# Kernel optimization log

Hardware: AMD Instinct MI355X
Metric: run time of the kernel (lower is better)

Reference implementation:

```python
import jax, jax.numpy as jnp
import numpy as np

C = 64; K = 3; KS = 7; A = 16
B, H, W = 4, 128, 128
EXTEND_SCOPE = 1.0
EPS = 1e-5

def _dct_mats(n):
    k = np.arange(n)[:, None]; m = np.arange(n)[None, :]
    D = 2.0 * np.cos(np.pi * (2 * m + 1) * k / (2.0 * n))  # torch_dct DCT-II, norm=None
    return jnp.asarray(D, jnp.float32), jnp.asarray(np.linalg.inv(D), jnp.float32)

_D, _Dinv = _dct_mats(K)

def _conv2d(x, w, b=None, stride=(1, 1), padding='SAME', groups=1):
    y = jax.lax.conv_general_dilated(x, w, stride, padding, feature_group_count=groups, dimension_numbers=('NCHW', 'OIHW', 'NCHW'))
    return y if b is None else y + b[None, :, None, None]

def _dwt(x):
    x1 = x[:, :, 0::2, 0::2] * 0.5; x2 = x[:, :, 1::2, 0::2] * 0.5
    x3 = x[:, :, 0::2, 1::2] * 0.5; x4 = x[:, :, 1::2, 1::2] * 0.5
    return (x1 + x2 + x3 + x4, -x1 + x2 - x3 + x4, -x1 - x2 + x3 + x4, x1 - x2 - x3 + x4)

def _iwt(LL, LH, HL, HH):
    a, b_, c, d = LL * 0.5, LH * 0.5, HL * 0.5, HH * 0.5
    n, ch, h, w = LL.shape
    out = jnp.zeros((n, ch, 2 * h, 2 * w), LL.dtype)
    out = out.at[:, :, 0::2, 0::2].set(a - b_ - c + d)
    out = out.at[:, :, 1::2, 0::2].set(a + b_ - c - d)
    out = out.at[:, :, 0::2, 1::2].set(a - b_ + c - d)
    out = out.at[:, :, 1::2, 1::2].set(a + b_ + c + d)
    return out

def _omni(x, fc_w, bn_g, bn_b, bn_m, bn_v, ch_w, ch_b, fl_w, fl_b, sp_w=None, sp_b=None):
    g = x.mean((2, 3))                                   # global avg pool -> [B,C]
    a = g @ fc_w.T
    a = jax.nn.relu((a - bn_m) * jax.lax.rsqrt(bn_v + EPS) * bn_g + bn_b)  # BN (eval)
    c_att = jax.nn.sigmoid(a @ ch_w.T + ch_b)
    f_att = jax.nn.sigmoid(a @ fl_w.T + fl_b)
    sp_att = None if sp_w is None else jax.nn.sigmoid(a @ sp_w.T + sp_b)
    return c_att, f_att, sp_att

def _forward(x, weight, ratio, o1_fc_w, o1_bn_g, o1_bn_b, o1_bn_m, o1_bn_v, o1_ch_w, o1_ch_b, o1_fl_w, o1_fl_b, o2_fc_w, o2_bn_g, o2_bn_b, o2_bn_m, o2_bn_v, o2_ch_w, o2_ch_b, o2_fl_w, o2_fl_b, o2_sp_w, o2_sp_b, off_w, off_b, obn_g, obn_b, obn_m, obn_v, ds_w, ds_b, gn_g, gn_b):
    b = x.shape[0]
    LL, LH, HL, HH = _dwt(x)
    c1, f1, _ = _omni(x, o1_fc_w, o1_bn_g, o1_bn_b, o1_bn_m, o1_bn_v, o1_ch_w, o1_ch_b, o1_fl_w, o1_fl_b)
    c2, f2, sp2 = _omni(x, o2_fc_w, o2_bn_g, o2_bn_b, o2_bn_m, o2_bn_v, o2_ch_w, o2_ch_b, o2_fl_w, o2_fl_b, o2_sp_w, o2_sp_b)
    # adaptive frequency-modulated dynamic kernels
    aw = jnp.broadcast_to(weight[None], (b,) + weight.shape)        # [B,Co,Ci,K,K]
    awm = aw.mean((-1, -2), keepdims=True)
    awr = aw - awm
    dctc = jnp.einsum('km,bojmn,ln->bojkl', _D, awr, _D)            # dct_2d
    dctc = dctc * (sp2.reshape(b, 1, 1, K, K) * 2.0)
    awr = jnp.einsum('km,bojmn,ln->bojkl', _Dinv, dctc, _Dinv)      # idct_2d
    aw = ratio * (awm * (c1[:, None, :, None, None] * 2) * (f1[:, :, None, None, None] * 2)) + (1.0 - ratio) * (awr * (c2[:, None, :, None, None] * 2) * (f2[:, :, None, None, None] * 2))
    # grouped conv (groups=b*C) then sum over c_in == depthwise conv with kernels summed over c_in (Cin==Cout)
    weff = aw.sum(axis=2)                                           # [B,C,K,K]
    h2, w2 = HH.shape[2], HH.shape[3]
    hh = _conv2d(HH.reshape(1, b * C, h2, w2), weff.reshape(b * C, 1, K, K), groups=b * C).reshape(b, C, h2, w2)
    out = _iwt(LL, LH, HL, hh) + x
    # ---- DSConv (dynamic snake conv, morph=0) ----
    off = _conv2d(out, off_w, off_b)
    off = (off - obn_m[None, :, None, None]) * jax.lax.rsqrt(obn_v + EPS)[None, :, None, None] * obn_g[None, :, None, None] + obn_b[None, :, None, None]
    y_off = jnp.tanh(off)[:, :KS]                                   # [B,KS,H,W]
    center = KS // 2
    low = jnp.flip(jnp.cumsum(jnp.flip(y_off[:, :center], 1), 1), 1)
    up = jnp.cumsum(y_off[:, center + 1:], 1)
    dy = jnp.concatenate([low, jnp.zeros_like(y_off[:, :1]), up], 1) * EXTEND_SCOPE
    hh_, ww_ = out.shape[2], out.shape[3]
    rows = jnp.clip(jnp.arange(hh_, dtype=x.dtype)[None, None, :, None] + dy, 0.0, hh_ - 1.0)
    cols = jnp.arange(ww_, dtype=x.dtype)[None, None, None, :] + (jnp.arange(KS, dtype=x.dtype) - center)[None, :, None, None]
    cols = jnp.clip(jnp.broadcast_to(cols, rows.shape), 0.0, ww_ - 1.0)
    r0 = jnp.floor(rows); c0 = jnp.floor(cols)
    wr = (rows - r0)[:, None]; wc = (cols - c0)[:, None]            # [B,1,KS,H,W]
    r0i = r0.astype(jnp.int32); c0i = c0.astype(jnp.int32)
    r1i = jnp.minimum(r0i + 1, hh_ - 1); c1i = jnp.minimum(c0i + 1, ww_ - 1)
    samp = jax.vmap(lambda img, ri, ci: img[:, ri, ci])             # [C,H,W],[KS,H,W] -> [C,KS,H,W]
    g00 = samp(out, r0i, c0i); g01 = samp(out, r0i, c1i)
    g10 = samp(out, r1i, c0i); g11 = samp(out, r1i, c1i)
    deform = (1 - wr) * (1 - wc) * g00 + (1 - wr) * wc * g01 + wr * (1 - wc) * g10 + wr * wc * g11
    deform = deform.transpose(0, 1, 3, 2, 4).reshape(b, C, hh_ * KS, ww_)
    y = _conv2d(deform, ds_w, ds_b, stride=(KS, 1), padding='VALID')  # [B,C,H,W]
    G = C // 4                                                       # GroupNorm(out//4)
    z = y.reshape(b, G, C // G, hh_, ww_)
    mu = z.mean((2, 3, 4), keepdims=True)
    var = ((z - mu) ** 2).mean((2, 3, 4), keepdims=True)
    y = ((z - mu) * jax.lax.rsqrt(var + EPS)).reshape(b, C, hh_, ww_)
    return jax.nn.relu(y * gn_g[None, :, None, None] + gn_b[None, :, None, None])

def setup_inputs() -> dict:
    key = jax.random.key(0)
    ks = jax.random.split(key, 12)
    def n(k, shape, s): return jax.random.normal(k, shape, jnp.float32) * s
    return dict(
        x=jax.random.normal(ks[0], (B, C, H, W), jnp.float32),
        weight=n(ks[1], (C, C, K, K), 0.1),
        ratio=jnp.asarray(0.5, jnp.float32),
        o1_fc_w=n(ks[2], (A, C), 0.2), o1_bn_g=jnp.ones((A,), jnp.float32), o1_bn_b=jnp.zeros((A,), jnp.float32),
        o1_bn_m=jnp.zeros((A,), jnp.float32), o1_bn_v=jnp.ones((A,), jnp.float32),
        o1_ch_w=n(ks[3], (C, A), 0.2), o1_ch_b=jnp.zeros((C,), jnp.float32),
        o1_fl_w=n(ks[4], (C, A), 0.2), o1_fl_b=jnp.zeros((C,), jnp.float32),
        o2_fc_w=n(ks[5], (A, C), 0.2), o2_bn_g=jnp.ones((A,), jnp.float32), o2_bn_b=jnp.zeros((A,), jnp.float32),
        o2_bn_m=jnp.zeros((A,), jnp.float32), o2_bn_v=jnp.ones((A,), jnp.float32),
        o2_ch_w=n(ks[6], (C, A), 0.2), o2_ch_b=jnp.zeros((C,), jnp.float32),
        o2_fl_w=n(ks[7], (C, A), 0.2), o2_fl_b=jnp.zeros((C,), jnp.float32),
        o2_sp_w=n(ks[8], (K * K, A), 0.2), o2_sp_b=jnp.zeros((K * K,), jnp.float32),
        off_w=n(ks[9], (2 * KS, C, 3, 3), 0.05), off_b=jnp.zeros((2 * KS,), jnp.float32),
        obn_g=jnp.ones((2 * KS,), jnp.float32), obn_b=jnp.zeros((2 * KS,), jnp.float32),
        obn_m=jnp.zeros((2 * KS,), jnp.float32), obn_v=jnp.ones((2 * KS,), jnp.float32),
        ds_w=n(ks[10], (C, C, KS, 1), 0.05), ds_b=jnp.zeros((C,), jnp.float32),
        gn_g=jnp.ones((C,), jnp.float32), gn_b=jnp.zeros((C,), jnp.float32),
    )

def reference(x, weight, ratio, o1_fc_w, o1_bn_g, o1_bn_b, o1_bn_m, o1_bn_v, o1_ch_w, o1_ch_b, o1_fl_w, o1_fl_b, o2_fc_w, o2_bn_g, o2_bn_b, o2_bn_m, o2_bn_v, o2_ch_w, o2_ch_b, o2_fl_w, o2_fl_b, o2_sp_w, o2_sp_b, off_w, off_b, obn_g, obn_b, obn_m, obn_v, ds_w, ds_b, gn_g, gn_b):
    return _forward(x, weight, ratio, o1_fc_w, o1_bn_g, o1_bn_b, o1_bn_m, o1_bn_v, o1_ch_w, o1_ch_b, o1_fl_w, o1_fl_b, o2_fc_w, o2_bn_g, o2_bn_b, o2_bn_m, o2_bn_v, o2_ch_w, o2_ch_b, o2_fl_w, o2_fl_b, o2_sp_w, o2_sp_b, off_w, off_b, obn_g, obn_b, obn_m, obn_v, ds_w, ds_b, gn_g, gn_b)
```

## Files before the change

### kernel.cpp

```cpp
#include <hip/hip_runtime.h>
#include <math.h>

#define BB 4
#define CC 64
#define HH_ 128
#define WW 128
#define HPW (HH_*WW)
#define KH 64
#define KW 64
#define KSZ 7
#define AA 16
#define EPSV 1e-5f
#define KTOT 448

typedef __attribute__((ext_vector_type(8))) short bf16x8;
typedef __attribute__((ext_vector_type(4))) float f32x4;
typedef unsigned short ushort_t;

__device__ __forceinline__ float sigm(float x){ return 1.0f/(1.0f+expf(-x)); }
__device__ __forceinline__ unsigned short f2bf(float f){
  unsigned u = __float_as_uint(f);
  return (unsigned short)((u + 0x7fffu + ((u>>16)&1u)) >> 16);
}

__global__ __launch_bounds__(512) void k_dwt0(const float* __restrict__ x,
  const float* __restrict__ dsw, const float* __restrict__ offw,
  float* __restrict__ HHb, float* __restrict__ partial,
  ushort_t* __restrict__ dsWbf, ushort_t* __restrict__ offAbf)
{
  int t = threadIdx.x; int wg = blockIdx.x;
  int idx = wg*512 + t;
  if(idx < CC*KTOT){
    int co = idx/KTOT; int K = idx%KTOT; int k = K>>6; int ci = K&63;
    dsWbf[idx] = f2bf(dsw[(size_t)(co*CC+ci)*KSZ + k]);
  } else {
    int j2 = idx - CC*KTOT;
    if(j2 < 18*16*32){
      int kl = j2&31; int co = (j2>>5)&15; int s = j2>>9;
      int tap = s>>1; int ci = (s&1)*32 + kl;
      float v = 0.f;
      if(co<KSZ) v = offw[((size_t)co*CC + ci)*9 + tap];
      offAbf[j2] = f2bf(v);
    }
  }
  int lane = t&63, wid = t>>6;
  int e0 = wg*2048 + t*4;
  int bc = e0>>12; int h2 = (e0>>6)&63; int w0 = e0&63;
  const float* xp = x + (size_t)bc*HPW;
  float4 a0 = *(const float4*)(xp + (2*h2)*WW + 2*w0);
  float4 a1 = *(const float4*)(xp + (2*h2)*WW + 2*w0 + 4);
  float4 b0 = *(const float4*)(xp + (2*h2+1)*WW + 2*w0);
  float4 b1 = *(const float4*)(xp + (2*h2+1)*WW + 2*w0 + 4);
  float4 hh;
  hh.x = 0.5f*(a0.x - b0.x - a0.y + b0.y);
  hh.y = 0.5f*(a0.z - b0.z - a0.w + b0.w);
  hh.z = 0.5f*(a1.x - b1.x - a1.y + b1.y);
  hh.w = 0.5f*(a1.z - b1.z - a1.w + b1.w);
  *(float4*)(HHb + e0) = hh;
  float s = a0.x+a0.y+a0.z+a0.w + a1.x+a1.y+a1.z+a1.w
          + b0.x+b0.y+b0.z+b0.w + b1.x+b1.y+b1.z+b1.w;
  for(int o=32;o>0;o>>=1) s += __shfl_down(s,o);
  __shared__ float ls[8];
  if(lane==0) ls[wid] = s;
  __syncthreads();
  if(t==0){
    float tot=0.f;
    #pragma unroll
    for(int k2=0;k2<8;k2++) tot += ls[k2];
    partial[wg] = tot;
  }
}

__global__ __launch_bounds__(64) void k_weff2(const float* __restrict__ partial,
  const float* __restrict__ w, const float* __restrict__ ratio_p,
  const float* __restrict__ o1fc, const float* __restrict__ o1g,const float* __restrict__ o1b,
  const float* __restrict__ o1m,const float* __restrict__ o1v,
  const float* __restrict__ o1cw,const float* __restrict__ o1cb,
  const float* __restrict__ o1fw,const float* __restrict__ o1fb,
  const float* __restrict__ o2fc, const float* __restrict__ o2g,const float* __restrict__ o2b,
  const float* __restrict__ o2m,const float* __restrict__ o2v,
  const float* __restrict__ o2cw,const float* __restrict__ o2cb,
  const float* __restrict__ o2fw,const float* __restrict__ o2fb,
  const float* __restrict__ spw,const float* __restrict__ spb,
  float* __restrict__ weff)
{
  int bo = blockIdx.x; int b = bo>>6, o = bo&63; int ci = threadIdx.x;
  int bc = b*CC+ci;
  float g_own = (partial[2*bc] + partial[2*bc+1]) * (1.0f/HPW);
  float d1=o1cb[ci], d2=o1fb[ci], d3=o2cb[ci], d4=o2fb[ci];
  float sspacc[9];
  #pragma unroll
  for(int e=0;e<9;e++) sspacc[e]=spb[e];
  for(int j=0;j<AA;j++){
    float p1 = g_own * o1fc[j*CC+ci];
    float p2 = g_own * o2fc[j*CC+ci];
    #pragma unroll
    for(int off=32;off>0;off>>=1){ p1+=__shfl_xor(p1,off); p2+=__shfl_xor(p2,off); }
    p1 = (p1-o1m[j])*rsqrtf(o1v[j]+EPSV)*o1g[j]+o1b[j]; p1=fmaxf(p1,0.f);
    p2 = (p2-o2m[j])*rsqrtf(o2v[j]+EPSV)*o2g[j]+o2b[j]; p2=fmaxf(p2,0.f);
    d1 += p1*o1cw[ci*AA+j]; d2 += p1*o1fw[ci*AA+j];
    d3 += p2*o2cw[ci*AA+j]; d4 += p2*o2fw[ci*AA+j];
    #pragma unroll
    for(int e=0;e<9;e++) sspacc[e] += p2*spw[e*AA+j];
  }
  float sc1v=sigm(d1), sc2v=sigm(d3);
  float sf1o=__shfl(sigm(d2),o), sf2o=__shfl(sigm(d4),o);
  const float* wp = w + (size_t)(o*CC+ci)*9;
  float w9[9]; float m=0.f;
  #pragma unroll
  for(int e=0;e<9;e++){ w9[e]=wp[e]; m+=w9[e]; }
  m *= (1.0f/9.0f);
  float S1 = m * sc1v;
  float M[9];
  #pragma unroll
  for(int e=0;e<9;e++) M[e] = (w9[e]-m)*sc2v;
  #pragma unroll
  for(int off=32; off>0; off>>=1){
    S1 += __shfl_xor(S1, off);
    #pragma unroll
    for(int e=0;e<9;e++) M[e] += __shfl_xor(M[e], off);
  }
  if(ci==0){
    const float Dm[3][3] = {{2.f,2.f,2.f},{1.7320508075688772f,0.f,-1.7320508075688772f},{1.f,-2.f,1.f}};
    const float Di[3][3] = {{0.16666666666666666f,0.28867513459481287f,0.16666666666666666f},
                            {0.16666666666666666f,0.f,-0.3333333333333333f},
                            {0.16666666666666666f,-0.28867513459481287f,0.16666666666666666f}};
    float U[3][3], T[3][3], V[3][3], R[3][3];
    for(int k=0;k<3;k++)for(int n=0;n<3;n++) U[k][n]=Dm[k][0]*M[0*3+n]+Dm[k][1]*M[1*3+n]+Dm[k][2]*M[2*3+n];
    for(int k=0;k<3;k++)for(int l=0;l<3;l++) T[k][l]=(U[k][0]*Dm[l][0]+U[k][1]*Dm[l][1]+U[k][2]*Dm[l][2])*2.0f*sigm(sspacc[k*3+l]);
    for(int k=0;k<3;k++)for(int n=0;n<3;n++) V[k][n]=Di[k][0]*T[0][n]+Di[k][1]*T[1][n]+Di[k][2]*T[2][n];
    for(int k=0;k<3;k++)for(int l=0;l<3;l++) R[k][l]=V[k][0]*Di[l][0]+V[k][1]*Di[l][1]+V[k][2]*Di[l][2];
    float rr = ratio_p[0];
    float base = rr*4.0f*sf1o*S1;
    float w2f = (1.0f-rr)*4.0f*sf2o;
    #pragma unroll
    for(int e=0;e<9;e++) weff[(size_t)bo*9+e] = base + w2f*R[e/3][e%3];
  }
}

__global__ __launch_bounds__(256) void k_iwtT(const float* __restrict__ HHb,
  const float* __restrict__ x, const float* __restrict__ weff,
  float* __restrict__ outT, ushort_t* __restrict__ outTbf)
{
  __shared__ __align__(16) char smem[33024 + 16640];
  float* hs  = (float*)smem;
  float* xt  = (float*)smem;
  float* d_s = (float*)(smem + 33024);
  int wg = blockIdx.x; int b = wg>>7, h = wg&127; int h2 = h>>1;
  int t = threadIdx.x;
  #pragma unroll
  for(int half=0; half<2; ++half){
    for(int e=t; e<32*3*66; e+=256){
      int c_l = e/198; int rem = e - c_l*198; int r3 = rem/66; int wz = rem - r3*66;
      int r = h2 - 1 + r3; int w2 = wz - 1;
      int c = half*32 + c_l;
      float v = 0.f;
      if(r>=0 && r<KH && w2>=0 && w2<KW)
        v = HHb[((size_t)(b*CC+c))*(KH*KW) + r*KW + w2];
      hs[(c_l*3 + r3)*66 + wz] = v;
    }
    __syncthreads();
    {
      int c_l = t>>3, q = t&7;
      int c = half*32 + c_l;
      float wk[9];
      #pragma unroll
      for(int e=0;e<9;e++) wk[e] = weff[(size_t)(b*CC+c)*9+e];
      const float* hb = hs + c_l*198;
      #pragma unroll
      for(int j=0;j<8;j++){
        int w2 = q*8+j;
        float conv = 0.f;
        #pragma unroll
        for(int dh=0;dh<3;dh++){
          const float* hr = hb + dh*66 + w2;
          conv += wk[dh*3+0]*hr[0] + wk[dh*3+1]*hr[1] + wk[dh*3+2]*hr[2];
        }
        d_s[c*65+w2] = 0.5f*(conv - hb[1*66 + w2 + 1]);
      }
    }
    __syncthreads();
  }
  for(int e=t; e<CC*WW; e+=256){
    int cc=e>>7, w=e&127;
    xt[cc*129+w] = x[((size_t)(b*CC+cc)*HH_+h)*WW + w];
  }
  __syncthreads();
  float* dst = outT + ((size_t)(b*HH_+h))*WW*CC;
  ushort_t* dstb = outTbf + ((size_t)(b*HH_+h))*130*CC;
  for(int e=t; e<CC*WW; e+=256){
    int w=e>>6, cc=e&63;
    float dv = d_s[cc*65+(w>>1)];
    float val = 2.f*xt[cc*129+w] + (((h + w)&1) ? -dv : dv);
    dst[e] = val;
    dstb[(w+1)*CC + cc] = f2bf(val);
  }
  if(t<128){ int cc=t&63; int side=t>>6; dstb[(size_t)side*129*CC + cc] = 0; }
}

__global__ __launch_bounds__(512) void k_dsfused(const float* __restrict__ outT,
  const ushort_t* __restrict__ outTbf, const ushort_t* __restrict__ dsWbf,
  const ushort_t* __restrict__ offAbf, const float* __restrict__ offb,
  const float* __restrict__ obg, const float* __restrict__ obb,
  const float* __restrict__ obm, const float* __restrict__ obv,
  const float* __restrict__ dsb, float* __restrict__ yout, float* __restrict__ pstats)
{
  __shared__ ushort_t S2a[2*8192];
  __shared__ int sb0[KSZ*128], sb1[KSZ*128];
  __shared__ float swr[KSZ*128];
  __shared__ float off_s[KSZ*128];
  __shared__ float dy_s[KSZ*128];
  int t = threadIdx.x;
  int wg = blockIdx.x; int sw = (wg&7)*64 + (wg>>3);
  int b = sw>>7, h = sw&127;
  int lane = t&63, wid = t>>6;
  int arow = lane&15, kgrp = lane>>4;
  {
    f32x4 acc = (f32x4){0.f,0.f,0.f,0.f};
    #pragma unroll
    for(int s=0;s<18;s++){
      int tap = s>>1, chalf = s&1;
      int r = tap/3, dwp = tap%3;
      int hr = h - 1 + r;
      if(hr<0 || hr>=HH_) continue;
      bf16x8 aF = *(const bf16x8*)(offAbf + (s*16+arow)*32 + kgrp*8);
      const ushort_t* base = outTbf + ((size_t)(b*HH_+hr))*130*CC + chalf*32 + kgrp*8;
      int wp = (wid<<4) + arow + dwp;
      bf16x8 bF = *(const bf16x8*)(base + (size_t)wp*CC);
      acc = __builtin_amdgcn_mfma_f32_16x16x32_bf16(aF, bF, acc, 0,0,0);
    }
    #pragma unroll
    for(int r=0;r<4;r++){
      int co = kgrp*4+r;
      if(co<KSZ) off_s[co*128 + (wid<<4) + arow] = acc[r];
    }
  }
  __syncthreads();
  if(t<128){
    int w = t;
    float y[KSZ];
    #pragma unroll
    for(int k=0;k<KSZ;k++){
      float sc = obg[k]*rsqrtf(obv[k]+EPSV);
      float sh = obb[k]-obm[k]*sc;
      y[k] = tanhf((off_s[k*128+w]+offb[k])*sc+sh);
    }
    dy_s[      w]=y[0]+y[1]+y[2]; dy_s[128+w]=y[1]+y[2]; dy_s[256+w]=y[2];
    dy_s[384+w]=0.f; dy_s[512+w]=y[4]; dy_s[640+w]=y[4]+y[5]; dy_s[768+w]=y[4]+y[5]+y[6];
  }
  __syncthreads();
  for(int e=t; e<KSZ*128; e+=512){
    int k = e>>7, w = e&127;
    float dv = dy_s[e];
    float r = fminf(fmaxf((float)h + dv, 0.f), 127.f);
    float rf = floorf(r); int r0=(int)rf; float wr=r-rf; int r1=min(r0+1,127);
    int c = min(max(w+k-3,0),127);
    sb0[k*128+w] = ((b*HH_+r0)*WW+c)*CC;
    sb1[k*128+w] = ((b*HH_+r1)*WW+c)*CC;
    swr[k*128+w] = wr;
  }
  __syncthreads();
  int cg2 = wid&3, wh = wid>>2;
  {
    ushort_t* buf = S2a;
    #pragma unroll
    for(int i=0;i<16;i++){
      int p = (wid<<4)+i;
      int b0=sb0[p], b1=sb1[p]; float wr=swr[p];
      float av = outT[b0+lane], c2 = outT[b1+lane];
      float v = av + wr*(c2-av);
      int idx = (p<<6)|lane;
      buf[idx ^ ((p&7)<<3)] = f2bf(v);
    }
  }
  __syncthreads();
  f32x4 acc[4];
  #pragma unroll
  for(int nt=0;nt<4;nt++) acc[nt] = (f32x4){0.f,0.f,0.f,0.f};
  int bufs = 0;
  for(int k=0;k<KSZ;k++){
    const ushort_t* Wp = dsWbf + (size_t)((cg2<<4)+arow)*KTOT + (k<<6) + kgrp*8;
    bf16x8 a0 = *(const bf16x8*)Wp;
    bf16x8 a1 = *(const bf16x8*)(Wp+32);
    if(k+1<KSZ){
      ushort_t* nb = S2a + (bufs^1)*8192;
      #pragma unroll
      for(int i=0;i<16;i++){
        int p = (wid<<4)+i;
        int b0=sb0[(k+1)*128+p], b1=sb1[(k+1)*128+p]; float wr=swr[(k+1)*128+p];
        float av = outT[b0+lane], c2 = outT[b1+lane];
        float v = av + wr*(c2-av);
        int idx = (p<<6)|lane;
        nb[idx ^ ((p&7)<<3)] = f2bf(v);
      }
    }
    const ushort_t* cb = S2a + bufs*8192;
    #pragma unroll
    for(int nt=0;nt<4;nt++){
      int pos = (wh<<6) + (nt<<4) + arow;
      int i0 = (pos<<6) + kgrp*8;
      int sz = (pos&7)<<3;
      bf16x8 b0 = *(const bf16x8*)(cb + (i0 ^ sz));
      bf16x8 b1 = *(const bf16x8*)(cb + ((i0+32) ^ sz));
      acc[nt] = __builtin_amdgcn_mfma_f32_16x16x32_bf16(a0, b0, acc[nt], 0,0,0);
      acc[nt] = __builtin_amdgcn_mfma_f32_16x16x32_bf16(a1, b1, acc[nt], 0,0,0);
    }
    __syncthreads();
    bufs ^= 1;
  }
  float vs[4]={0.f,0.f,0.f,0.f}, vq[4]={0.f,0.f,0.f,0.f};
  #pragma unroll
  for(int r=0;r<4;r++){
    int co = (cg2<<4) + kgrp*4 + r;
    float bias = dsb[co];
    #pragma unroll
    for(int nt=0;nt<4;nt++){
      float y = acc[nt][r] + bias;
      int wcol = (wh<<6) + (nt<<4) + arow;
      yout[((size_t)(b*CC+co)*HH_ + h)*WW + wcol] = y;
      vs[r] += y; vq[r] += y*y;
    }
  }
  #pragma unroll
  for(int m=1;m<16;m<<=1){
    #pragma unroll
    for(int r=0;r<4;r++){ vs[r]+=__shfl_xor(vs[r],m); vq[r]+=__shfl_xor(vq[r],m); }
  }
  if(arow==0){
    #pragma unroll
    for(int r=0;r<4;r++){
      int co = (cg2<<4)+kgrp*4+r;
      int pi = (b*CC+co)*256 + h*2 + wh;
      pstats[pi] = vs[r];
      pstats[65536+pi] = vq[r];
    }
  }
}

__global__ __launch_bounds__(256) void k_gnfin2(const float* __restrict__ pstats,
                                                float* __restrict__ gstat){
  int bg = blockIdx.x; int b = bg>>4, g = bg&15; int t = threadIdx.x;
  float s=0.f, q=0.f;
  #pragma unroll
  for(int c4=0;c4<4;c4++){
    int base = (b*CC + g*4+c4)*256;
    s += pstats[base + t];
    q += pstats[65536 + base + t];
  }
  for(int o=32;o>0;o>>=1){ s+=__shfl_down(s,o); q+=__shfl_down(q,o); }
  __shared__ float ls[4], lq[4];
  if((t&63)==0){ ls[t>>6]=s; lq[t>>6]=q; }
  __syncthreads();
  if(t==0){
    float S=ls[0]+ls[1]+ls[2]+ls[3], Q=lq[0]+lq[1]+lq[2]+lq[3];
    float inv = 1.0f/(4.0f*HPW);
    float mu = S*inv; float var = Q*inv - mu*mu;
    gstat[bg*2]=mu; gstat[bg*2+1]=rsqrtf(var+EPSV);
  }
}

__global__ void k_gnapply(float* __restrict__ y, const float* __restrict__ gstat,
  const float* __restrict__ gg, const float* __restrict__ gb){
  int idx = blockIdx.x*256 + threadIdx.x;
  float4* p = (float4*)y;
  int bc = idx >> 12;
  int b = bc>>6, c = bc&63;
  int gi = b*16 + (c>>2);
  float mu = gstat[gi*2], rstd = gstat[gi*2+1];
  float sc = rstd*gg[c], sh = gb[c]-mu*sc;
  float4 v = p[idx];
  v.x = fmaxf(v.x*sc+sh, 0.f);
  v.y = fmaxf(v.y*sc+sh, 0.f);
  v.z = fmaxf(v.z*sc+sh, 0.f);
  v.w = fmaxf(v.w*sc+sh, 0.f);
  p[idx] = v;
}

extern "C" void kernel_launch(void* const* d_in, const int* in_sizes, int n_in,
                              void* d_out, int out_size, void* d_ws, size_t ws_size,
                              hipStream_t stream) {
  const float* x      = (const float*)d_in[0];
  const float* weight = (const float*)d_in[1];
  const float* ratio  = (const float*)d_in[2];
  const float* o1fc   = (const float*)d_in[3];
  const float* o1g    = (const float*)d_in[4];
  const float* o1b    = (const float*)d_in[5];
  const float* o1m    = (const float*)d_in[6];
  const float* o1v    = (const float*)d_in[7];
  const float* o1cw   = (const float*)d_in[8];
  const float* o1cb   = (const float*)d_in[9];
  const float* o1fw   = (const float*)d_in[10];
  const float* o1fb   = (const float*)d_in[11];
  const float* o2fc   = (const float*)d_in[12];
  const float* o2g    = (const float*)d_in[13];
  const float* o2b    = (const float*)d_in[14];
  const float* o2m    = (const float*)d_in[15];
  const float* o2v    = (const float*)d_in[16];
  const float* o2cw   = (const float*)d_in[17];
  const float* o2cb   = (const float*)d_in[18];
  const float* o2fw   = (const float*)d_in[19];
  const float* o2fb   = (const float*)d_in[20];
  const float* spw    = (const float*)d_in[21];
  const float* spb    = (const float*)d_in[22];
  const float* offw   = (const float*)d_in[23];
  const float* offb   = (const float*)d_in[24];
  const float* obg    = (const float*)d_in[25];
  const float* obb    = (const float*)d_in[26];
  const float* obm    = (const float*)d_in[27];
  const float* obv    = (const float*)d_in[28];
  const float* dsw    = (const float*)d_in[29];
  const float* dsb    = (const float*)d_in[30];
  const float* gng    = (const float*)d_in[31];
  const float* gnb    = (const float*)d_in[32];

  float* ws    = (float*)d_ws;
  float* HHb   = ws;
  float* partial = ws + 1048576;
  float* weff  = ws + 1049088;
  float* gstat = ws + 1051392;
  ushort_t* dsWbf  = (ushort_t*)(ws + 1051520);
  ushort_t* offAbf = (ushort_t*)(ws + 1065856);
  float* pstats= ws + 1070464;
  float* outT  = ws + 1201536;
  ushort_t* outTbf = (ushort_t*)(ws + 5395840);
  float* outb  = (float*)d_out;

  k_dwt0<<<512,512,0,stream>>>(x, dsw, offw, HHb, partial, dsWbf, offAbf);
  k_weff2<<<256,64,0,stream>>>(partial, weight, ratio,
    o1fc,o1g,o1b,o1m,o1v,o1cw,o1cb,o1fw,o1fb,
    o2fc,o2g,o2b,o2m,o2v,o2cw,o2cb,o2fw,o2fb,
    spw,spb, weff);
  k_iwtT<<<512,256,0,stream>>>(HHb, x, weff, outT, outTbf);
  k_dsfused<<<512,512,0,stream>>>(outT, outTbf, dsWbf, offAbf,
    offb, obg, obb, obm, obv, dsb, outb, pstats);
  k_gnfin2<<<64,256,0,stream>>>(pstats, gstat);
  k_gnapply<<<4096,256,0,stream>>>(outb, gstat, gng, gnb);
}
```

Measured before the change: 95.87 us.

## Share IWT row pair per block and prefetch gathers into registers across MFMA

k_iwtT now handles both output rows that share one half-resolution HH row, so the 3x3 conv on HH is computed once per pair instead of twice, and the grid is halved. In k_dsfused, all 14 weight fragments are loaded into registers up front. The next tap's gathered outT values are issued as register loads before the MFMA block and only interpolated and written to LDS afterwards, so global load latency overlaps with matrix math. In exchange, register pressure rises (aF[14], L0/L1[16]) under a 512-thread launch bound that now also requests 4 blocks.

Result: slower. 101.9 us (+6.3%).

```diff
diff --git a/kernel.cpp b/kernel.cpp
--- a/kernel.cpp
+++ b/kernel.cpp
@@ -146,7 +146,7 @@
   float* hs  = (float*)smem;
   float* xt  = (float*)smem;
   float* d_s = (float*)(smem + 33024);
-  int wg = blockIdx.x; int b = wg>>7, h = wg&127; int h2 = h>>1;
+  int wg = blockIdx.x; int b = wg>>6, h2 = wg&63;
   int t = threadIdx.x;
   #pragma unroll
   for(int half=0; half<2; ++half){
@@ -181,24 +181,29 @@
     }
     __syncthreads();
   }
-  for(int e=t; e<CC*WW; e+=256){
-    int cc=e>>7, w=e&127;
-    xt[cc*129+w] = x[((size_t)(b*CC+cc)*HH_+h)*WW + w];
-  }
-  __syncthreads();
-  float* dst = outT + ((size_t)(b*HH_+h))*WW*CC;
-  ushort_t* dstb = outTbf + ((size_t)(b*HH_+h))*130*CC;
-  for(int e=t; e<CC*WW; e+=256){
-    int w=e>>6, cc=e&63;
-    float dv = d_s[cc*65+(w>>1)];
-    float val = 2.f*xt[cc*129+w] + (((h + w)&1) ? -dv : dv);
-    dst[e] = val;
-    dstb[(w+1)*CC + cc] = f2bf(val);
-  }
-  if(t<128){ int cc=t&63; int side=t>>6; dstb[(size_t)side*129*CC + cc] = 0; }
-}
-
-__global__ __launch_bounds__(512) void k_dsfused(const float* __restrict__ outT,
+  #pragma unroll
+  for(int r=0;r<2;r++){
+    int h = 2*h2 + r;
+    for(int e=t; e<CC*WW; e+=256){
+      int cc=e>>7, w=e&127;
+      xt[cc*129+w] = x[((size_t)(b*CC+cc)*HH_+h)*WW + w];
+    }
+    __syncthreads();
+    float* dst = outT + ((size_t)(b*HH_+h))*WW*CC;
+    ushort_t* dstb = outTbf + ((size_t)(b*HH_+h))*130*CC;
+    for(int e=t; e<CC*WW; e+=256){
+      int w=e>>6, cc=e&63;
+      float dv = d_s[cc*65+(w>>1)];
+      float val = 2.f*xt[cc*129+w] + (((h + w)&1) ? -dv : dv);
+      dst[e] = val;
+      dstb[(w+1)*CC + cc] = f2bf(val);
+    }
+    if(t<128){ int cc=t&63; int side=t>>6; dstb[(size_t)side*129*CC + cc] = 0; }
+    __syncthreads();
+  }
+}
+
+__global__ __launch_bounds__(512,4) void k_dsfused(const float* __restrict__ outT,
   const ushort_t* __restrict__ outTbf, const ushort_t* __restrict__ dsWbf,
   const ushort_t* __restrict__ offAbf, const float* __restrict__ offb,
   const float* __restrict__ obg, const float* __restrict__ obb,
@@ -261,17 +266,22 @@
   }
   __syncthreads();
   int cg2 = wid&3, wh = wid>>2;
+  int pbase = wid<<4;
+  bf16x8 aF[14];
   {
-    ushort_t* buf = S2a;
-    #pragma unroll
-    for(int i=0;i<16;i++){
-      int p = (wid<<4)+i;
-      int b0=sb0[p], b1=sb1[p]; float wr=swr[p];
-      float av = outT[b0+lane], c2 = outT[b1+lane];
-      float v = av + wr*(c2-av);
-      int idx = (p<<6)|lane;
-      buf[idx ^ ((p&7)<<3)] = f2bf(v);
-    }
+    const ushort_t* Wp = dsWbf + (size_t)((cg2<<4)+arow)*KTOT + kgrp*8;
+    #pragma unroll
+    for(int ks=0;ks<14;ks++) aF[ks] = *(const bf16x8*)(Wp + ks*32);
+  }
+  float L0[16], L1[16];
+  #pragma unroll
+  for(int i=0;i<16;i++){ int p=pbase+i; L0[i]=outT[sb0[p]+lane]; L1[i]=outT[sb1[p]+lane]; }
+  #pragma unroll
+  for(int i=0;i<16;i++){
+    int p=pbase+i;
+    float v = L0[i] + swr[p]*(L1[i]-L0[i]);
+    int idx=(p<<6)|lane;
+    S2a[idx ^ ((p&7)<<3)] = f2bf(v);
   }
   __syncthreads();
   f32x4 acc[4];
@@ -279,19 +289,11 @@
   for(int nt=0;nt<4;nt++) acc[nt] = (f32x4){0.f,0.f,0.f,0.f};
   int bufs = 0;
   for(int k=0;k<KSZ;k++){
-    const ushort_t* Wp = dsWbf + (size_t)((cg2<<4)+arow)*KTOT + (k<<6) + kgrp*8;
-    bf16x8 a0 = *(const bf16x8*)Wp;
-    bf16x8 a1 = *(const bf16x8*)(Wp+32);
     if(k+1<KSZ){
-      ushort_t* nb = S2a + (bufs^1)*8192;
       #pragma unroll
       for(int i=0;i<16;i++){
-        int p = (wid<<4)+i;
-        int b0=sb0[(k+1)*128+p], b1=sb1[(k+1)*128+p]; float wr=swr[(k+1)*128+p];
-        float av = outT[b0+lane], c2 = outT[b1+lane];
-        float v = av + wr*(c2-av);
-        int idx = (p<<6)|lane;
-        nb[idx ^ ((p&7)<<3)] = f2bf(v);
+        int e=(k+1)*128 + pbase + i;
+        L0[i]=outT[sb0[e]+lane]; L1[i]=outT[sb1[e]+lane];
       }
     }
     const ushort_t* cb = S2a + bufs*8192;
@@ -302,8 +304,18 @@
       int sz = (pos&7)<<3;
       bf16x8 b0 = *(const bf16x8*)(cb + (i0 ^ sz));
       bf16x8 b1 = *(const bf16x8*)(cb + ((i0+32) ^ sz));
-      acc[nt] = __builtin_amdgcn_mfma_f32_16x16x32_bf16(a0, b0, acc[nt], 0,0,0);
-      acc[nt] = __builtin_amdgcn_mfma_f32_16x16x32_bf16(a1, b1, acc[nt], 0,0,0);
+      acc[nt] = __builtin_amdgcn_mfma_f32_16x16x32_bf16(aF[2*k], b0, acc[nt], 0,0,0);
+      acc[nt] = __builtin_amdgcn_mfma_f32_16x16x32_bf16(aF[2*k+1], b1, acc[nt], 0,0,0);
+    }
+    if(k+1<KSZ){
+      ushort_t* nb = S2a + (bufs^1)*8192;
+      #pragma unroll
+      for(int i=0;i<16;i++){
+        int p = pbase+i;
+        float v = L0[i] + swr[(k+1)*128+p]*(L1[i]-L0[i]);
+        int idx=(p<<6)|lane;
+        nb[idx ^ ((p&7)<<3)] = f2bf(v);
+      }
     }
     __syncthreads();
     bufs ^= 1;
@@ -430,7 +442,7 @@
     o1fc,o1g,o1b,o1m,o1v,o1cw,o1cb,o1fw,o1fb,
     o2fc,o2g,o2b,o2m,o2v,o2cw,o2cb,o2fw,o2fb,
     spw,spb, weff);
-  k_iwtT<<<512,256,0,stream>>>(HHb, x, weff, outT, outTbf);
+  k_iwtT<<<256,256,0,stream>>>(HHb, x, weff, outT, outTbf);
   k_dsfused<<<512,512,0,stream>>>(outT, outTbf, dsWbf, offAbf,
     offb, obg, obb, obm, obv, dsb, outb, pstats);
   k_gnfin2<<<64,256,0,stream>>>(pstats, gstat);
```

## Gather deformable samples directly into MFMA registers and halve iwt blocks

Applied to the files above, without the earlier changes.

The deformable-conv kernel no longer stages interpolated samples in a double-buffered LDS tile with barriers. Each wave now loads float4 vectors from outT for its own 16 columns, lerps them straight into bf16 MFMA B fragments, and loops over all four output-channel groups. This drops shared memory traffic and per-tap syncs, but each wave now reloads all the weight fragments and the partial-stats buffer grows fourfold. Separately, the iwt kernel handles two output rows per block, reusing the HH conv result (d_s) for both rows instead of recomputing it per row.

Result: slower. 135.5 us (+41.3%).

```diff
diff --git a/kernel.cpp b/kernel.cpp
--- a/kernel.cpp
+++ b/kernel.cpp
@@ -21,6 +21,18 @@
 __device__ __forceinline__ unsigned short f2bf(float f){
   unsigned u = __float_as_uint(f);
   return (unsigned short)((u + 0x7fffu + ((u>>16)&1u)) >> 16);
+}
+__device__ __forceinline__ bf16x8 lerp8(float4 a0, float4 a1, float4 b0, float4 b1, float wr){
+  bf16x8 r;
+  r[0]=(short)f2bf(a0.x + wr*(b0.x-a0.x));
+  r[1]=(short)f2bf(a0.y + wr*(b0.y-a0.y));
+  r[2]=(short)f2bf(a0.z + wr*(b0.z-a0.z));
+  r[3]=(short)f2bf(a0.w + wr*(b0.w-a0.w));
+  r[4]=(short)f2bf(a1.x + wr*(b1.x-a1.x));
+  r[5]=(short)f2bf(a1.y + wr*(b1.y-a1.y));
+  r[6]=(short)f2bf(a1.z + wr*(b1.z-a1.z));
+  r[7]=(short)f2bf(a1.w + wr*(b1.w-a1.w));
+  return r;
 }
 
 __global__ __launch_bounds__(512) void k_dwt0(const float* __restrict__ x,
@@ -146,7 +158,7 @@
   float* hs  = (float*)smem;
   float* xt  = (float*)smem;
   float* d_s = (float*)(smem + 33024);
-  int wg = blockIdx.x; int b = wg>>7, h = wg&127; int h2 = h>>1;
+  int wg = blockIdx.x; int b = wg>>6, h2 = wg&63;
   int t = threadIdx.x;
   #pragma unroll
   for(int half=0; half<2; ++half){
@@ -181,21 +193,26 @@
     }
     __syncthreads();
   }
-  for(int e=t; e<CC*WW; e+=256){
-    int cc=e>>7, w=e&127;
-    xt[cc*129+w] = x[((size_t)(b*CC+cc)*HH_+h)*WW + w];
-  }
-  __syncthreads();
-  float* dst = outT + ((size_t)(b*HH_+h))*WW*CC;
-  ushort_t* dstb = outTbf + ((size_t)(b*HH_+h))*130*CC;
-  for(int e=t; e<CC*WW; e+=256){
-    int w=e>>6, cc=e&63;
-    float dv = d_s[cc*65+(w>>1)];
-    float val = 2.f*xt[cc*129+w] + (((h + w)&1) ? -dv : dv);
-    dst[e] = val;
-    dstb[(w+1)*CC + cc] = f2bf(val);
-  }
-  if(t<128){ int cc=t&63; int side=t>>6; dstb[(size_t)side*129*CC + cc] = 0; }
+  #pragma unroll
+  for(int r=0;r<2;r++){
+    int h = 2*h2 + r;
+    for(int e=t; e<CC*WW; e+=256){
+      int cc=e>>7, w=e&127;
+      xt[cc*129+w] = x[((size_t)(b*CC+cc)*HH_+h)*WW + w];
+    }
+    __syncthreads();
+    float* dst = outT + ((size_t)(b*HH_+h))*WW*CC;
+    ushort_t* dstb = outTbf + ((size_t)(b*HH_+h))*130*CC;
+    for(int e=t; e<CC*WW; e+=256){
+      int w=e>>6, cc=e&63;
+      float dv = d_s[cc*65+(w>>1)];
+      float val = 2.f*xt[cc*129+w] + (((h + w)&1) ? -dv : dv);
+      dst[e] = val;
+      dstb[(w+1)*CC + cc] = f2bf(val);
+    }
+    if(t<128){ int cc=t&63; int side=t>>6; dstb[(size_t)side*129*CC + cc] = 0; }
+    __syncthreads();
+  }
 }
 
 __global__ __launch_bounds__(512) void k_dsfused(const float* __restrict__ outT,
@@ -205,7 +222,6 @@
   const float* __restrict__ obm, const float* __restrict__ obv,
   const float* __restrict__ dsb, float* __restrict__ yout, float* __restrict__ pstats)
 {
-  __shared__ ushort_t S2a[2*8192];
   __shared__ int sb0[KSZ*128], sb1[KSZ*128];
   __shared__ float swr[KSZ*128];
   __shared__ float off_s[KSZ*128];
@@ -260,79 +276,65 @@
     swr[k*128+w] = wr;
   }
   __syncthreads();
-  int cg2 = wid&3, wh = wid>>2;
-  {
-    ushort_t* buf = S2a;
-    #pragma unroll
-    for(int i=0;i<16;i++){
-      int p = (wid<<4)+i;
-      int b0=sb0[p], b1=sb1[p]; float wr=swr[p];
-      float av = outT[b0+lane], c2 = outT[b1+lane];
-      float v = av + wr*(c2-av);
-      int idx = (p<<6)|lane;
-      buf[idx ^ ((p&7)<<3)] = f2bf(v);
-    }
-  }
-  __syncthreads();
+  int w = (wid<<4) + arow;
   f32x4 acc[4];
   #pragma unroll
-  for(int nt=0;nt<4;nt++) acc[nt] = (f32x4){0.f,0.f,0.f,0.f};
-  int bufs = 0;
+  for(int cg=0;cg<4;cg++) acc[cg] = (f32x4){0.f,0.f,0.f,0.f};
+  #pragma unroll
   for(int k=0;k<KSZ;k++){
-    const ushort_t* Wp = dsWbf + (size_t)((cg2<<4)+arow)*KTOT + (k<<6) + kgrp*8;
-    bf16x8 a0 = *(const bf16x8*)Wp;
-    bf16x8 a1 = *(const bf16x8*)(Wp+32);
-    if(k+1<KSZ){
-      ushort_t* nb = S2a + (bufs^1)*8192;
+    int e = k*128 + w;
+    int b0 = sb0[e], b1 = sb1[e]; float wr = swr[e];
+    int off = kgrp*8;
+    const float* p0 = outT + b0 + off;
+    const float* p1 = outT + b1 + off;
+    const float* q0 = p0 + 32;
+    const float* q1 = p1 + 32;
+    float4 r0a = *(const float4*)(p0);
+    float4 r0b = *(const float4*)(p0+4);
+    float4 r1a = *(const float4*)(p1);
+    float4 r1b = *(const float4*)(p1+4);
+    float4 s0a = *(const float4*)(q0);
+    float4 s0b = *(const float4*)(q0+4);
+    float4 s1a = *(const float4*)(q1);
+    float4 s1b = *(const float4*)(q1+4);
+    bf16x8 bF0 = lerp8(r0a, r0b, r1a, r1b, wr);
+    bf16x8 bF1 = lerp8(s0a, s0b, s1a, s1b, wr);
+    #pragma unroll
+    for(int cg=0;cg<4;cg++){
+      const ushort_t* Wp = dsWbf + (size_t)((cg<<4)+arow)*KTOT + (k<<6) + kgrp*8;
+      bf16x8 a0 = *(const bf16x8*)Wp;
+      bf16x8 a1 = *(const bf16x8*)(Wp+32);
+      acc[cg] = __builtin_amdgcn_mfma_f32_16x16x32_bf16(a0, bF0, acc[cg], 0,0,0);
+      acc[cg] = __builtin_amdgcn_mfma_f32_16x16x32_bf16(a1, bF1, acc[cg], 0,0,0);
+    }
+  }
+  float vs[16], vq[16];
+  #pragma unroll
+  for(int cg=0;cg<4;cg++){
+    #pragma unroll
+    for(int r=0;r<4;r++){
+      int co = (cg<<4) + kgrp*4 + r;
+      float y = acc[cg][r] + dsb[co];
+      int wcol = (wid<<4) + arow;
+      yout[((size_t)(b*CC+co)*HH_ + h)*WW + wcol] = y;
+      vs[cg*4+r] = y; vq[cg*4+r] = y*y;
+    }
+  }
+  #pragma unroll
+  for(int m=1;m<16;m<<=1){
+    #pragma unroll
+    for(int i=0;i<16;i++){ vs[i]+=__shfl_xor(vs[i],m); vq[i]+=__shfl_xor(vq[i],m); }
+  }
+  if(arow==0){
+    #pragma unroll
+    for(int cg=0;cg<4;cg++){
       #pragma unroll
-      for(int i=0;i<16;i++){
-        int p = (wid<<4)+i;
-        int b0=sb0[(k+1)*128+p], b1=sb1[(k+1)*128+p]; float wr=swr[(k+1)*128+p];
-        float av = outT[b0+lane], c2 = outT[b1+lane];
-        float v = av + wr*(c2-av);
-        int idx = (p<<6)|lane;
-        nb[idx ^ ((p&7)<<3)] = f2bf(v);
+      for(int r=0;r<4;r++){
+        int co = (cg<<4)+kgrp*4+r;
+        int pi = (b*CC+co)*1024 + h*8 + wid;
+        pstats[pi] = vs[cg*4+r];
+        pstats[262144+pi] = vq[cg*4+r];
       }
-    }
-    const ushort_t* cb = S2a + bufs*8192;
-    #pragma unroll
-    for(int nt=0;nt<4;nt++){
-      int pos = (wh<<6) + (nt<<4) + arow;
-      int i0 = (pos<<6) + kgrp*8;
-      int sz = (pos&7)<<3;
-      bf16x8 b0 = *(const bf16x8*)(cb + (i0 ^ sz));
-      bf16x8 b1 = *(const bf16x8*)(cb + ((i0+32) ^ sz));
-      acc[nt] = __builtin_amdgcn_mfma_f32_16x16x32_bf16(a0, b0, acc[nt], 0,0,0);
-      acc[nt] = __builtin_amdgcn_mfma_f32_16x16x32_bf16(a1, b1, acc[nt], 0,0,0);
-    }
-    __syncthreads();
-    bufs ^= 1;
-  }
-  float vs[4]={0.f,0.f,0.f,0.f}, vq[4]={0.f,0.f,0.f,0.f};
-  #pragma unroll
-  for(int r=0;r<4;r++){
-    int co = (cg2<<4) + kgrp*4 + r;
-    float bias = dsb[co];
-    #pragma unroll
-    for(int nt=0;nt<4;nt++){
-      float y = acc[nt][r] + bias;
-      int wcol = (wh<<6) + (nt<<4) + arow;
-      yout[((size_t)(b*CC+co)*HH_ + h)*WW + wcol] = y;
-      vs[r] += y; vq[r] += y*y;
-    }
-  }
-  #pragma unroll
-  for(int m=1;m<16;m<<=1){
-    #pragma unroll
-    for(int r=0;r<4;r++){ vs[r]+=__shfl_xor(vs[r],m); vq[r]+=__shfl_xor(vq[r],m); }
-  }
-  if(arow==0){
-    #pragma unroll
-    for(int r=0;r<4;r++){
-      int co = (cg2<<4)+kgrp*4+r;
-      int pi = (b*CC+co)*256 + h*2 + wh;
-      pstats[pi] = vs[r];
-      pstats[65536+pi] = vq[r];
     }
   }
 }
@@ -343,9 +345,11 @@
   float s=0.f, q=0.f;
   #pragma unroll
   for(int c4=0;c4<4;c4++){
-    int base = (b*CC + g*4+c4)*256;
-    s += pstats[base + t];
-    q += pstats[65536 + base + t];
+    int base = (b*CC + g*4+c4)*1024;
+    for(int i=t;i<1024;i+=256){
+      s += pstats[base + i];
+      q += pstats[262144 + base + i];
+    }
   }
   for(int o=32;o>0;o>>=1){ s+=__shfl_down(s,o); q+=__shfl_down(q,o); }
   __shared__ float ls[4], lq[4];
@@ -421,8 +425,8 @@
   ushort_t* dsWbf  = (ushort_t*)(ws + 1051520);
   ushort_t* offAbf = (ushort_t*)(ws + 1065856);
   float* pstats= ws + 1070464;
-  float* outT  = ws + 1201536;
-  ushort_t* outTbf = (ushort_t*)(ws + 5395840);
+  float* outT  = ws + 1594752;
+  ushort_t* outTbf = (ushort_t*)(ws + 5789056);
   float* outb  = (float*)d_out;
 
   k_dwt0<<<512,512,0,stream>>>(x, dsw, offw, HHb, partial, dsWbf, offAbf);
@@ -430,7 +434,7 @@
     o1fc,o1g,o1b,o1m,o1v,o1cw,o1cb,o1fw,o1fb,
     o2fc,o2g,o2b,o2m,o2v,o2cw,o2cb,o2fw,o2fb,
     spw,spb, weff);
-  k_iwtT<<<512,256,0,stream>>>(HHb, x, weff, outT, outTbf);
+  k_iwtT<<<256,256,0,stream>>>(HHb, x, weff, outT, outTbf);
   k_dsfused<<<512,512,0,stream>>>(outT, outTbf, dsWbf, offAbf,
     offb, obg, obb, obm, obv, dsb, outb, pstats);
   k_gnfin2<<<64,256,0,stream>>>(pstats, gstat);
```

## Split deformable-conv blocks by width half and share HH-conv across row pairs

Applied to the files above, without the earlier changes.

k_iwtT now handles two output rows per block, so the 3x3 conv on the half-resolution HH band is computed once and reused for both rows instead of being recomputed. k_dsfused is split into 1024 blocks of 256 threads, each covering a 64-column half-row with 4 waves that each own 16 output channels, and it preloads all 14 weight fragments into registers before the k-loop. The aim is to remove redundant conv work, raise block count and occupancy for the fused kernel, and take weight loads out of the inner loop. The cost is that the offset conv and gather are duplicated per half-row, and register pressure rises from holding 14 bf16x8 fragments.

Measured after the change: 108.4 us. +13.1%, slower.

```diff
diff --git a/kernel.cpp b/kernel.cpp
--- a/kernel.cpp
+++ b/kernel.cpp
@@ -146,7 +146,7 @@
   float* hs  = (float*)smem;
   float* xt  = (float*)smem;
   float* d_s = (float*)(smem + 33024);
-  int wg = blockIdx.x; int b = wg>>7, h = wg&127; int h2 = h>>1;
+  int wg = blockIdx.x; int b = wg>>6, h2 = wg&63;
   int t = threadIdx.x;
   #pragma unroll
   for(int half=0; half<2; ++half){
@@ -181,38 +181,44 @@
     }
     __syncthreads();
   }
-  for(int e=t; e<CC*WW; e+=256){
-    int cc=e>>7, w=e&127;
-    xt[cc*129+w] = x[((size_t)(b*CC+cc)*HH_+h)*WW + w];
-  }
-  __syncthreads();
-  float* dst = outT + ((size_t)(b*HH_+h))*WW*CC;
-  ushort_t* dstb = outTbf + ((size_t)(b*HH_+h))*130*CC;
-  for(int e=t; e<CC*WW; e+=256){
-    int w=e>>6, cc=e&63;
-    float dv = d_s[cc*65+(w>>1)];
-    float val = 2.f*xt[cc*129+w] + (((h + w)&1) ? -dv : dv);
-    dst[e] = val;
-    dstb[(w+1)*CC + cc] = f2bf(val);
-  }
-  if(t<128){ int cc=t&63; int side=t>>6; dstb[(size_t)side*129*CC + cc] = 0; }
-}
-
-__global__ __launch_bounds__(512) void k_dsfused(const float* __restrict__ outT,
+  #pragma unroll
+  for(int r=0;r<2;r++){
+    int h = 2*h2 + r;
+    for(int e=t; e<CC*WW; e+=256){
+      int cc=e>>7, w=e&127;
+      xt[cc*129+w] = x[((size_t)(b*CC+cc)*HH_+h)*WW + w];
+    }
+    __syncthreads();
+    float* dst = outT + ((size_t)(b*HH_+h))*WW*CC;
+    ushort_t* dstb = outTbf + ((size_t)(b*HH_+h))*130*CC;
+    for(int e=t; e<CC*WW; e+=256){
+      int w=e>>6, cc=e&63;
+      float dv = d_s[cc*65+(w>>1)];
+      float val = 2.f*xt[cc*129+w] + (((h + w)&1) ? -dv : dv);
+      dst[e] = val;
+      dstb[(w+1)*CC + cc] = f2bf(val);
+    }
+    if(t<128){ int cc=t&63; int side=t>>6; dstb[(size_t)side*129*CC + cc] = 0; }
+    __syncthreads();
+  }
+}
+
+__global__ __launch_bounds__(256) void k_dsfused(const float* __restrict__ outT,
   const ushort_t* __restrict__ outTbf, const ushort_t* __restrict__ dsWbf,
   const ushort_t* __restrict__ offAbf, const float* __restrict__ offb,
   const float* __restrict__ obg, const float* __restrict__ obb,
   const float* __restrict__ obm, const float* __restrict__ obv,
   const float* __restrict__ dsb, float* __restrict__ yout, float* __restrict__ pstats)
 {
-  __shared__ ushort_t S2a[2*8192];
-  __shared__ int sb0[KSZ*128], sb1[KSZ*128];
-  __shared__ float swr[KSZ*128];
-  __shared__ float off_s[KSZ*128];
-  __shared__ float dy_s[KSZ*128];
+  __shared__ ushort_t S2a[2*4096];
+  __shared__ int sb0[KSZ*64], sb1[KSZ*64];
+  __shared__ float swr[KSZ*64];
+  __shared__ float off_s[KSZ*64];
+  __shared__ float dy_s[KSZ*64];
   int t = threadIdx.x;
-  int wg = blockIdx.x; int sw = (wg&7)*64 + (wg>>3);
-  int b = sw>>7, h = sw&127;
+  int wg = blockIdx.x;
+  int sw = (wg&7)*128 + (wg>>3);
+  int b = sw>>8, h = (sw>>1)&127, wseg = sw&1;
   int lane = t&63, wid = t>>6;
   int arow = lane&15, kgrp = lane>>4;
   {
@@ -225,42 +231,48 @@
       if(hr<0 || hr>=HH_) continue;
       bf16x8 aF = *(const bf16x8*)(offAbf + (s*16+arow)*32 + kgrp*8);
       const ushort_t* base = outTbf + ((size_t)(b*HH_+hr))*130*CC + chalf*32 + kgrp*8;
-      int wp = (wid<<4) + arow + dwp;
+      int wp = wseg*64 + (wid<<4) + arow + dwp;
       bf16x8 bF = *(const bf16x8*)(base + (size_t)wp*CC);
       acc = __builtin_amdgcn_mfma_f32_16x16x32_bf16(aF, bF, acc, 0,0,0);
     }
     #pragma unroll
     for(int r=0;r<4;r++){
       int co = kgrp*4+r;
-      if(co<KSZ) off_s[co*128 + (wid<<4) + arow] = acc[r];
-    }
-  }
-  __syncthreads();
-  if(t<128){
-    int w = t;
+      if(co<KSZ) off_s[co*64 + (wid<<4) + arow] = acc[r];
+    }
+  }
+  __syncthreads();
+  if(t<64){
+    int wl = t;
     float y[KSZ];
     #pragma unroll
     for(int k=0;k<KSZ;k++){
       float sc = obg[k]*rsqrtf(obv[k]+EPSV);
       float sh = obb[k]-obm[k]*sc;
-      y[k] = tanhf((off_s[k*128+w]+offb[k])*sc+sh);
-    }
-    dy_s[      w]=y[0]+y[1]+y[2]; dy_s[128+w]=y[1]+y[2]; dy_s[256+w]=y[2];
-    dy_s[384+w]=0.f; dy_s[512+w]=y[4]; dy_s[640+w]=y[4]+y[5]; dy_s[768+w]=y[4]+y[5]+y[6];
-  }
-  __syncthreads();
-  for(int e=t; e<KSZ*128; e+=512){
-    int k = e>>7, w = e&127;
+      y[k] = tanhf((off_s[k*64+wl]+offb[k])*sc+sh);
+    }
+    dy_s[     wl]=y[0]+y[1]+y[2]; dy_s[64+wl]=y[1]+y[2]; dy_s[128+wl]=y[2];
+    dy_s[192+wl]=0.f; dy_s[256+wl]=y[4]; dy_s[320+wl]=y[4]+y[5]; dy_s[384+wl]=y[4]+y[5]+y[6];
+  }
+  __syncthreads();
+  for(int e=t; e<KSZ*64; e+=256){
+    int k = e>>6, wl = e&63;
+    int w = wseg*64 + wl;
     float dv = dy_s[e];
     float r = fminf(fmaxf((float)h + dv, 0.f), 127.f);
     float rf = floorf(r); int r0=(int)rf; float wr=r-rf; int r1=min(r0+1,127);
     int c = min(max(w+k-3,0),127);
-    sb0[k*128+w] = ((b*HH_+r0)*WW+c)*CC;
-    sb1[k*128+w] = ((b*HH_+r1)*WW+c)*CC;
-    swr[k*128+w] = wr;
-  }
-  __syncthreads();
-  int cg2 = wid&3, wh = wid>>2;
+    sb0[e] = ((b*HH_+r0)*WW+c)*CC;
+    sb1[e] = ((b*HH_+r1)*WW+c)*CC;
+    swr[e] = wr;
+  }
+  __syncthreads();
+  bf16x8 aF[14];
+  {
+    const ushort_t* Wp = dsWbf + (size_t)((wid<<4)+arow)*KTOT + kgrp*8;
+    #pragma unroll
+    for(int ks=0;ks<14;ks++) aF[ks] = *(const bf16x8*)(Wp + ks*32);
+  }
   {
     ushort_t* buf = S2a;
     #pragma unroll
@@ -279,31 +291,29 @@
   for(int nt=0;nt<4;nt++) acc[nt] = (f32x4){0.f,0.f,0.f,0.f};
   int bufs = 0;
   for(int k=0;k<KSZ;k++){
-    const ushort_t* Wp = dsWbf + (size_t)((cg2<<4)+arow)*KTOT + (k<<6) + kgrp*8;
-    bf16x8 a0 = *(const bf16x8*)Wp;
-    bf16x8 a1 = *(const bf16x8*)(Wp+32);
     if(k+1<KSZ){
-      ushort_t* nb = S2a + (bufs^1)*8192;
+      ushort_t* nb = S2a + (bufs^1)*4096;
       #pragma unroll
       for(int i=0;i<16;i++){
         int p = (wid<<4)+i;
-        int b0=sb0[(k+1)*128+p], b1=sb1[(k+1)*128+p]; float wr=swr[(k+1)*128+p];
+        int e = (k+1)*64 + p;
+        int b0=sb0[e], b1=sb1[e]; float wr=swr[e];
         float av = outT[b0+lane], c2 = outT[b1+lane];
         float v = av + wr*(c2-av);
         int idx = (p<<6)|lane;
         nb[idx ^ ((p&7)<<3)] = f2bf(v);
       }
     }
-    const ushort_t* cb = S2a + bufs*8192;
+    const ushort_t* cb = S2a + bufs*4096;
     #pragma unroll
     for(int nt=0;nt<4;nt++){
-      int pos = (wh<<6) + (nt<<4) + arow;
+      int pos = (nt<<4) + arow;
       int i0 = (pos<<6) + kgrp*8;
       int sz = (pos&7)<<3;
       bf16x8 b0 = *(const bf16x8*)(cb + (i0 ^ sz));
       bf16x8 b1 = *(const bf16x8*)(cb + ((i0+32) ^ sz));
-      acc[nt] = __builtin_amdgcn_mfma_f32_16x16x32_bf16(a0, b0, acc[nt], 0,0,0);
-      acc[nt] = __builtin_amdgcn_mfma_f32_16x16x32_bf16(a1, b1, acc[nt], 0,0,0);
+      acc[nt] = __builtin_amdgcn_mfma_f32_16x16x32_bf16(aF[2*k], b0, acc[nt], 0,0,0);
+      acc[nt] = __builtin_amdgcn_mfma_f32_16x16x32_bf16(aF[2*k+1], b1, acc[nt], 0,0,0);
     }
     __syncthreads();
     bufs ^= 1;
@@ -311,12 +321,12 @@
   float vs[4]={0.f,0.f,0.f,0.f}, vq[4]={0.f,0.f,0.f,0.f};
   #pragma unroll
   for(int r=0;r<4;r++){
-    int co = (cg2<<4) + kgrp*4 + r;
+    int co = (wid<<4) + kgrp*4 + r;
     float bias = dsb[co];
     #pragma unroll
     for(int nt=0;nt<4;nt++){
       float y = acc[nt][r] + bias;
-      int wcol = (wh<<6) + (nt<<4) + arow;
+      int wcol = wseg*64 + (nt<<4) + arow;
       yout[((size_t)(b*CC+co)*HH_ + h)*WW + wcol] = y;
       vs[r] += y; vq[r] += y*y;
     }
@@ -329,8 +339,8 @@
   if(arow==0){
     #pragma unroll
     for(int r=0;r<4;r++){
-      int co = (cg2<<4)+kgrp*4+r;
-      int pi = (b*CC+co)*256 + h*2 + wh;
+      int co = (wid<<4)+kgrp*4+r;
+      int pi = (b*CC+co)*256 + h*2 + wseg;
       pstats[pi] = vs[r];
       pstats[65536+pi] = vq[r];
     }
@@ -430,8 +440,8 @@
     o1fc,o1g,o1b,o1m,o1v,o1cw,o1cb,o1fw,o1fb,
     o2fc,o2g,o2b,o2m,o2v,o2cw,o2cb,o2fw,o2fb,
     spw,spb, weff);
-  k_iwtT<<<512,256,0,stream>>>(HHb, x, weff, outT, outTbf);
-  k_dsfused<<<512,512,0,stream>>>(outT, outTbf, dsWbf, offAbf,
+  k_iwtT<<<256,256,0,stream>>>(HHb, x, weff, outT, outTbf);
+  k_dsfused<<<1024,256,0,stream>>>(outT, outTbf, dsWbf, offAbf,
     offb, obg, obb, obm, obv, dsb, outb, pstats);
   k_gnfin2<<<64,256,0,stream>>>(pstats, gstat);
   k_gnapply<<<4096,256,0,stream>>>(outb, gstat, gng, gnb);
```
